# Performance work log

Hardware: AMD Instinct MI355X
Metric: run time of the kernel (lower is better)

The kernel has to match this reference:

```python
import jax, jax.numpy as jnp
import numpy as np

SIMILAR_GROUPS = ['\u0131i', 'o\u00f6', 'u\u00fc', 'g\u011f']  # iı, oö, uü, gğ

def _group_table(vocab):
    # group id per codepoint: 0 = not in any similar-chars group
    tbl = np.zeros((vocab,), dtype=np.int32)
    for gid, chars in enumerate(SIMILAR_GROUPS, start=1):
        for c in chars:
            if ord(c) < vocab:
                tbl[ord(c)] = gid
    return jnp.asarray(tbl)

def setup_inputs() -> dict:
    key = jax.random.key(0)
    k1, k2 = jax.random.split(key)
    N, V = 524288, 512
    pred = jax.random.normal(k1, (N, V), dtype=jnp.float32)
    target = jax.random.randint(k2, (N,), 0, V, dtype=jnp.int64)
    return {"pred": pred, "target": target}

def reference(pred, target):
    V = pred.shape[-1]
    group = _group_table(V)
    # per-element cross entropy: -log_softmax(pred)[i, target[i]]
    logp = jax.nn.log_softmax(pred, axis=-1)
    base_loss = -jnp.take_along_axis(logp, target[:, None], axis=-1)[:, 0]
    # predicted class (codepoint) and Turkish similar-char group match
    pred_chars = jnp.argmax(pred, axis=-1)
    gp = group[pred_chars]
    gt = group[target]
    # original: p_char must be a dict key (gp>0) and t_char in its group string
    scale = jnp.where((gp > 0) & (gp == gt), jnp.float32(0.8), jnp.float32(1.0))
    return jnp.mean(base_loss * scale)
```

## Files before the change

### kernel.cpp

```cpp
#include <hip/hip_runtime.h>


#define V 512

__device__ __forceinline__ int grp(int c) {
    if (c == 105 || c == 305) return 1;
    if (c == 111 || c == 246) return 2;
    if (c == 117 || c == 252) return 3;
    if (c == 103 || c == 287) return 4;
    return 0;
}

__global__ __launch_bounds__(256) void turkish_loss_kernel(
    const float* __restrict__ pred, const int* __restrict__ target,
    float* __restrict__ ws_sum, int N)
{
    __shared__ float wave_part[4];
    const int lane  = threadIdx.x & 63;
    const int wid   = threadIdx.x >> 6;
    const int gwave = blockIdx.x * 4 + wid;
    const int nwave = gridDim.x * 4;

    float acc = 0.0f;

    for (int row = gwave; row < N; row += nwave) {
        const float4* p = (const float4*)(pred + (size_t)row * V);
        float4 a = p[lane];
        float4 b = p[64 + lane];
        float v[8] = {a.x, a.y, a.z, a.w, b.x, b.y, b.z, b.w};
        const int base0 = 4 * lane;
        const int base1 = 256 + 4 * lane;

        float m = v[0]; int mi = base0;
        #pragma unroll
        for (int j = 1; j < 4; ++j)
            if (v[j] > m) { m = v[j]; mi = base0 + j; }
        #pragma unroll
        for (int j = 0; j < 4; ++j)
            if (v[4 + j] > m) { m = v[4 + j]; mi = base1 + j; }

        #pragma unroll
        for (int off = 1; off < 64; off <<= 1) {
            float m2 = __shfl_xor(m, off);
            int   i2 = __shfl_xor(mi, off);
            if (m2 > m || (m2 == m && i2 < mi)) { m = m2; mi = i2; }
        }

        const int t = target[row];
        float s = 0.0f, tv = 0.0f;
        #pragma unroll
        for (int j = 0; j < 4; ++j) {
            s += __expf(v[j] - m);
            tv += (base0 + j == t) ? v[j] : 0.0f;
        }
        #pragma unroll
        for (int j = 0; j < 4; ++j) {
            s += __expf(v[4 + j] - m);
            tv += (base1 + j == t) ? v[4 + j] : 0.0f;
        }
        #pragma unroll
        for (int off = 1; off < 64; off <<= 1) {
            s  += __shfl_xor(s, off);
            tv += __shfl_xor(tv, off);
        }

        if (lane == 0) {
            float loss = m + __logf(s) - tv;
            int gp = grp(mi), gt = grp(t);
            float scale = (gp > 0 && gp == gt) ? 0.8f : 1.0f;
            acc += loss * scale;
        }
    }

    if (lane == 0) wave_part[wid] = acc;
    __syncthreads();
    if (threadIdx.x == 0) {
        float bsum = wave_part[0] + wave_part[1] + wave_part[2] + wave_part[3];
        atomicAdd(ws_sum, bsum);
    }
}

__global__ void turkish_loss_finalize(const float* __restrict__ ws_sum,
                                      float* __restrict__ out, float invN)
{
    out[0] = ws_sum[0] * invN;
}

extern "C" void kernel_launch(void* const* d_in, const int* in_sizes, int n_in,
                              void* d_out, int out_size, void* d_ws, size_t ws_size,
                              hipStream_t stream) {
    const float* pred   = (const float*)d_in[0];
    const int*   target = (const int*)d_in[1];
    const int N = in_sizes[1];
    float* ws_sum = (float*)d_ws;

    hipMemsetAsync(d_ws, 0, sizeof(float), stream);

    turkish_loss_kernel<<<dim3(2048), dim3(256), 0, stream>>>(pred, target, ws_sum, N);
    turkish_loss_finalize<<<1, 1, 0, stream>>>(ws_sum, (float*)d_out, 1.0f / (float)N);
}
```

Baseline: 1.366 ms.

## Process four rows per wave with 16-lane groups and direct target load

Each wave now handles four rows concurrently, with a 16-lane subgroup per row. Each lane loads eight float4 values per row, and the target logit is read directly instead of being found through a masked reduction. This cuts the wave-wide shuffle reductions from six steps to four and drops the target-value reduction, while increasing the loads in flight per wave. Register use rises because each lane now holds 32 floats.

Result: no change. 1.343 ms (-1.7%).

```diff
diff --git a/kernel.cpp b/kernel.cpp
--- a/kernel.cpp
+++ b/kernel.cpp
@@ -16,62 +16,62 @@
     float* __restrict__ ws_sum, int N)
 {
     __shared__ float wave_part[4];
-    const int lane  = threadIdx.x & 63;
-    const int wid   = threadIdx.x >> 6;
-    const int gwave = blockIdx.x * 4 + wid;
-    const int nwave = gridDim.x * 4;
+    const int lane = threadIdx.x & 63;
+    const int wid  = threadIdx.x >> 6;
+    const int sub  = lane >> 4;
+    const int gl   = lane & 15;
+    const int gquad = blockIdx.x * 4 + wid;
+    const int nquad = gridDim.x * 4;
 
     float acc = 0.0f;
 
-    for (int row = gwave; row < N; row += nwave) {
-        const float4* p = (const float4*)(pred + (size_t)row * V);
-        float4 a = p[lane];
-        float4 b = p[64 + lane];
-        float v[8] = {a.x, a.y, a.z, a.w, b.x, b.y, b.z, b.w};
-        const int base0 = 4 * lane;
-        const int base1 = 256 + 4 * lane;
+    for (int q = gquad; (q << 2) < N; q += nquad) {
+        int row = (q << 2) + sub;
+        const bool valid = row < N;
+        if (!valid) row = 0;
+        const float* rp = pred + (size_t)row * V;
+        const int t = target[row];
+        const float tv = rp[t];
+        float4 d[8];
+        const float4* p4 = (const float4*)rp;
+        #pragma unroll
+        for (int k = 0; k < 8; ++k) d[k] = p4[gl + 16 * k];
 
-        float m = v[0]; int mi = base0;
+        float m = d[0].x; int mi = 4 * gl;
         #pragma unroll
-        for (int j = 1; j < 4; ++j)
-            if (v[j] > m) { m = v[j]; mi = base0 + j; }
-        #pragma unroll
-        for (int j = 0; j < 4; ++j)
-            if (v[4 + j] > m) { m = v[4 + j]; mi = base1 + j; }
+        for (int k = 0; k < 8; ++k) {
+            const float vv[4] = {d[k].x, d[k].y, d[k].z, d[k].w};
+            #pragma unroll
+            for (int j = 0; j < 4; ++j) {
+                const int col = 64 * k + 4 * gl + j;
+                if (vv[j] > m) { m = vv[j]; mi = col; }
+            }
+        }
 
         #pragma unroll
-        for (int off = 1; off < 64; off <<= 1) {
-            float m2 = __shfl_xor(m, off);
-            int   i2 = __shfl_xor(mi, off);
+        for (int off = 1; off < 16; off <<= 1) {
+            const float m2 = __shfl_xor(m, off);
+            const int   i2 = __shfl_xor(mi, off);
             if (m2 > m || (m2 == m && i2 < mi)) { m = m2; mi = i2; }
         }
 
-        const int t = target[row];
-        float s = 0.0f, tv = 0.0f;
+        float s = 0.0f;
         #pragma unroll
-        for (int j = 0; j < 4; ++j) {
-            s += __expf(v[j] - m);
-            tv += (base0 + j == t) ? v[j] : 0.0f;
-        }
+        for (int k = 0; k < 8; ++k)
+            s += __expf(d[k].x - m) + __expf(d[k].y - m)
+               + __expf(d[k].z - m) + __expf(d[k].w - m);
         #pragma unroll
-        for (int j = 0; j < 4; ++j) {
-            s += __expf(v[4 + j] - m);
-            tv += (base1 + j == t) ? v[4 + j] : 0.0f;
-        }
-        #pragma unroll
-        for (int off = 1; off < 64; off <<= 1) {
-            s  += __shfl_xor(s, off);
-            tv += __shfl_xor(tv, off);
-        }
+        for (int off = 1; off < 16; off <<= 1) s += __shfl_xor(s, off);
 
-        if (lane == 0) {
-            float loss = m + __logf(s) - tv;
-            int gp = grp(mi), gt = grp(t);
-            float scale = (gp > 0 && gp == gt) ? 0.8f : 1.0f;
-            acc += loss * scale;
+        if (gl == 0 && valid) {
+            const float loss = m + __logf(s) - tv;
+            const int gp = grp(mi), gt = grp(t);
+            acc += loss * ((gp > 0 && gp == gt) ? 0.8f : 1.0f);
         }
     }
 
+    acc += __shfl_xor(acc, 16);
+    acc += __shfl_xor(acc, 32);
     if (lane == 0) wave_part[wid] = acc;
     __syncthreads();
     if (threadIdx.x == 0) {
```
